# Kernel optimization log

Measured on AMD Instinct MI355X. Metric: run time of the kernel, lower is better.

The kernel has to match this reference:

```python
import jax, jax.numpy as jnp
import numpy as np

DIM = 1024
HEADS = 16
DIM_HEAD = 64
INNER = HEADS * DIM_HEAD  # 1024


def setup_inputs() -> dict:
    key = jax.random.key(0)
    kx, kqkv, kwo, kbo = jax.random.split(key, 4)
    x = jax.random.normal(kx, (4, 2048, DIM), dtype=jnp.float32)
    # nn.Linear weights stored as [out, in]; we keep [in, out] for x @ W
    w_qkv = jax.random.normal(kqkv, (DIM, 3 * INNER), dtype=jnp.float32) * (1.0 / np.sqrt(DIM))
    w_out = jax.random.normal(kwo, (INNER, DIM), dtype=jnp.float32) * (1.0 / np.sqrt(INNER))
    b_out = jax.random.normal(kbo, (DIM,), dtype=jnp.float32) * 0.01
    return {"x": x, "w_qkv": w_qkv, "w_out": w_out, "b_out": b_out}


def reference(x, w_qkv, w_out, b_out):
    b, n, _ = x.shape
    scale = 1.0 / np.sqrt(DIM_HEAD)
    qkv = x @ w_qkv  # [b, n, 3*inner]
    q, k, v = jnp.split(qkv, 3, axis=-1)
    # [b, n, inner] -> [b, h, n, d]
    reshape = lambda z: z.reshape(b, n, HEADS, DIM_HEAD).transpose(0, 2, 1, 3)
    q, k, v = reshape(q), reshape(k), reshape(v)
    sim = jnp.einsum('bhid,bhjd->bhij', q, k) * scale
    attn = jax.nn.softmax(sim, axis=-1)  # dropout p=0.0 -> identity
    out = jnp.einsum('bhij,bhjd->bhid', attn, v)
    out = out.transpose(0, 2, 1, 3).reshape(b, n, INNER)
    return out @ w_out + b_out
```

## Files before the change

### kernel.cpp

```cpp
#include <hip/hip_runtime.h>
#include <hip/hip_fp16.h>

typedef __attribute__((ext_vector_type(4))) float f32x4;
typedef __attribute__((ext_vector_type(8))) _Float16 h8;
typedef __attribute__((ext_vector_type(4))) _Float16 h4;
typedef __attribute__((ext_vector_type(2))) _Float16 h2;
typedef __attribute__((ext_vector_type(2))) __fp16 fp16x2;

__device__ __forceinline__ void gld16(const _Float16* g, _Float16* l) {
  __builtin_amdgcn_global_load_lds(
      (const __attribute__((address_space(1))) void*)g,
      (__attribute__((address_space(3))) void*)l, 16, 0, 0);
}

__device__ __forceinline__ h4 pack4(float p0, float p1, float p2, float p3) {
  fp16x2 lo = __builtin_amdgcn_cvt_pkrtz(p0, p1);
  fp16x2 hi = __builtin_amdgcn_cvt_pkrtz(p2, p3);
  h2 lo2 = __builtin_bit_cast(h2, lo);
  h2 hi2 = __builtin_bit_cast(h2, hi);
  return __builtin_shufflevector(lo2, hi2, 0, 1, 2, 3);
}

__global__ void cvt_f32_h(const float* __restrict__ in, _Float16* __restrict__ out, int n8) {
  for (int i = blockIdx.x * blockDim.x + threadIdx.x; i < n8; i += gridDim.x * blockDim.x) {
    const f32x4* p = (const f32x4*)(in + (size_t)i * 8);
    f32x4 a = p[0], b = p[1];
    h8 o;
    o[0] = (_Float16)a[0]; o[1] = (_Float16)a[1]; o[2] = (_Float16)a[2]; o[3] = (_Float16)a[3];
    o[4] = (_Float16)b[0]; o[5] = (_Float16)b[1]; o[6] = (_Float16)b[2]; o[7] = (_Float16)b[3];
    *(h8*)(out + (size_t)i * 8) = o;
  }
}

__global__ void transpose_cvt(const float* __restrict__ in, _Float16* __restrict__ out, int R, int C) {
  __shared__ float tile[32][33];
  const int tx = threadIdx.x & 31, ty = threadIdx.x >> 5;
  const int c = blockIdx.x * 32 + tx;
#pragma unroll
  for (int j = 0; j < 32; j += 8) {
    int r = blockIdx.y * 32 + ty + j;
    tile[ty + j][tx] = in[(size_t)r * C + c];
  }
  __syncthreads();
#pragma unroll
  for (int j = 0; j < 32; j += 8) {
    out[(size_t)(blockIdx.x * 32 + ty + j) * R + blockIdx.y * 32 + tx] = (_Float16)tile[tx][ty + j];
  }
}

template <int EPI>
__global__ __launch_bounds__(256, 2)
void gemm_kernel(const _Float16* __restrict__ A, const _Float16* __restrict__ Bt,
                 float* __restrict__ outF, const float* __restrict__ bias,
                 _Float16* __restrict__ q_h, _Float16* __restrict__ k_h,
                 _Float16* __restrict__ v_t, const int Nn, const int K) {
  __shared__ _Float16 As[128 * 64];
  __shared__ _Float16 Bs[128 * 64];
  const int tid = threadIdx.x;
  const int wid = tid >> 6, lane = tid & 63;
  const int g = lane >> 4, r16 = lane & 15;
  const int wr = wid >> 1, wc = wid & 1;
  const int row0 = blockIdx.x * 128;
  const int col0 = blockIdx.y * 128;
  f32x4 acc[4][4] = {};
  const int sr = tid >> 3, sc = tid & 7;
  const _Float16* ag = A + (size_t)(row0 + sr) * K + sc * 8;
  const _Float16* bg = Bt + (size_t)(col0 + sr) * K + sc * 8;

  for (int kt = 0; kt < K; kt += 64) {
    __syncthreads();
#pragma unroll
    for (int i = 0; i < 4; ++i)
      gld16(ag + (size_t)i * 32 * K + kt, As + i * 2048 + wid * 512);
#pragma unroll
    for (int i = 0; i < 4; ++i)
      gld16(bg + (size_t)i * 32 * K + kt, Bs + i * 2048 + wid * 512);
    __syncthreads();

#pragma unroll
    for (int kk = 0; kk < 2; ++kk) {
      h8 af[4], bf[4];
#pragma unroll
      for (int mt = 0; mt < 4; ++mt)
        af[mt] = *(const h8*)(As + (wr * 64 + mt * 16 + r16) * 64 + kk * 32 + g * 8);
#pragma unroll
      for (int nt = 0; nt < 4; ++nt)
        bf[nt] = *(const h8*)(Bs + (wc * 64 + nt * 16 + r16) * 64 + kk * 32 + g * 8);
#pragma unroll
      for (int mt = 0; mt < 4; ++mt)
#pragma unroll
        for (int nt = 0; nt < 4; ++nt)
          acc[mt][nt] = __builtin_amdgcn_mfma_f32_16x16x32_f16(af[mt], bf[nt], acc[mt][nt], 0, 0, 0);
    }
  }

  if (EPI == 0) {
    const float qscale = 0.125f * 1.44269504088896340736f;
#pragma unroll
    for (int mt = 0; mt < 4; ++mt) {
#pragma unroll
      for (int nt = 0; nt < 4; ++nt) {
        const int j = col0 + wc * 64 + nt * 16 + r16;
        const int which = j >> 10;
        const int hd = j & 1023;
        const int hh = hd >> 6, dd = hd & 63;
#pragma unroll
        for (int rg = 0; rg < 4; ++rg) {
          const int mm = row0 + wr * 64 + mt * 16 + g * 4 + rg;
          const int b = mm >> 11, n = mm & 2047;
          const size_t bh = (size_t)(b * 16 + hh);
          const float v = acc[mt][nt][rg];
          if (which == 0)      q_h[(bh * 2048 + n) * 64 + dd] = (_Float16)(v * qscale);
          else if (which == 1) k_h[(bh * 2048 + n) * 64 + dd] = (_Float16)v;
          else                 v_t[(bh * 64 + dd) * 2048 + n] = (_Float16)v;
        }
      }
    }
  } else {
#pragma unroll
    for (int mt = 0; mt < 4; ++mt) {
#pragma unroll
      for (int nt = 0; nt < 4; ++nt) {
        const int j = col0 + wc * 64 + nt * 16 + r16;
        const float bv = bias[j];
#pragma unroll
        for (int rg = 0; rg < 4; ++rg) {
          const int mm = row0 + wr * 64 + mt * 16 + g * 4 + rg;
          outF[(size_t)mm * Nn + j] = acc[mt][nt][rg] + bv;
        }
      }
    }
  }
}

__device__ __forceinline__ void stage_kv(const _Float16* Kg, const _Float16* Vg,
                                         _Float16* KsB, _Float16* VsB,
                                         int kv0, int sr, int sc8, int wid) {
#pragma unroll
  for (int i = 0; i < 2; ++i) {
    int r = i * 32 + sr;
    gld16(Kg + (size_t)(kv0 + r) * 64 + (sc8 ^ ((r & 7) * 8)), KsB + i * 2048 + wid * 512);
    gld16(Vg + (size_t)r * 2048 + kv0 + (sc8 ^ ((r & 7) * 8)), VsB + i * 2048 + wid * 512);
  }
}

__global__ __launch_bounds__(256, 2)
void attn_kernel(const _Float16* __restrict__ Qall, const _Float16* __restrict__ Kall,
                 const _Float16* __restrict__ Vtall, _Float16* __restrict__ Oall) {
  __shared__ _Float16 Qs[256 * 64];
  __shared__ _Float16 Ks[2][64 * 64];
  __shared__ _Float16 Vs[2][64 * 64];
  const int tid = threadIdx.x;
  const int wid = tid >> 6, lane = tid & 63;
  const int g = lane >> 4, r16 = lane & 15;
  const int blk = (blockIdx.x & 7) * 64 + (blockIdx.x >> 3);
  const int qt = blk & 7;
  const int bh = blk >> 3;
  const _Float16* Qg = Qall + (size_t)bh * (2048 * 64);
  const _Float16* Kg = Kall + (size_t)bh * (2048 * 64);
  const _Float16* Vg = Vtall + (size_t)bh * (2048 * 64);
  const int q0 = qt * 256;
  const int sr = tid >> 3, sc8 = (tid & 7) * 8;

#pragma unroll
  for (int i = 0; i < 8; ++i) {
    int r = i * 32 + sr;
    gld16(Qg + (size_t)(q0 + r) * 64 + (sc8 ^ ((r & 7) * 8)), Qs + i * 2048 + wid * 512);
  }
  stage_kv(Kg, Vg, Ks[0], Vs[0], 0, sr, sc8, wid);
  __syncthreads();

  h8 qf[4][2];
#pragma unroll
  for (int qb = 0; qb < 4; ++qb) {
    const int qrow = wid * 64 + qb * 16 + r16;
#pragma unroll
    for (int kd = 0; kd < 2; ++kd)
      qf[qb][kd] = *(const h8*)(Qs + qrow * 64 + ((kd * 32 + g * 8) ^ ((qrow & 7) * 8)));
  }

  f32x4 ot[4][4] = {};
  f32x4 lacc[4] = {};
  float m[4];
#pragma unroll
  for (int qb = 0; qb < 4; ++qb) m[qb] = -3.0e38f;
  const h4 ones = {(_Float16)1.f, (_Float16)1.f, (_Float16)1.f, (_Float16)1.f};

  auto compute = [&](const _Float16* KsB, const _Float16* VsB) {
    h8 kf[4][2];
#pragma unroll
    for (int kb = 0; kb < 4; ++kb) {
      const int krow = kb * 16 + r16;
#pragma unroll
      for (int kd = 0; kd < 2; ++kd)
        kf[kb][kd] = *(const h8*)(KsB + krow * 64 + ((kd * 32 + g * 8) ^ ((krow & 7) * 8)));
    }
    h4 vf[4][4];
#pragma unroll
    for (int db = 0; db < 4; ++db) {
      const int vrow = db * 16 + r16;
#pragma unroll
      for (int kg = 0; kg < 4; ++kg)
        vf[db][kg] = *(const h4*)(VsB + vrow * 64 + ((kg * 16 + g * 4) ^ ((vrow & 7) * 8)));
    }
#pragma unroll
    for (int qb = 0; qb < 4; ++qb) {
      f32x4 st[4];
#pragma unroll
      for (int kb = 0; kb < 4; ++kb) {
        f32x4 z = {};
        st[kb] = __builtin_amdgcn_mfma_f32_16x16x32_f16(kf[kb][0], qf[qb][0], z, 0, 0, 0);
      }
#pragma unroll
      for (int kb = 0; kb < 4; ++kb)
        st[kb] = __builtin_amdgcn_mfma_f32_16x16x32_f16(kf[kb][1], qf[qb][1], st[kb], 0, 0, 0);

      float a0 = fmaxf(fmaxf(st[0][0], st[0][1]), fmaxf(st[0][2], st[0][3]));
      float a1 = fmaxf(fmaxf(st[1][0], st[1][1]), fmaxf(st[1][2], st[1][3]));
      float a2 = fmaxf(fmaxf(st[2][0], st[2][1]), fmaxf(st[2][2], st[2][3]));
      float a3 = fmaxf(fmaxf(st[3][0], st[3][1]), fmaxf(st[3][2], st[3][3]));
      float pmax = fmaxf(fmaxf(a0, a1), fmaxf(a2, a3));
      pmax = fmaxf(pmax, __shfl_xor(pmax, 16));
      pmax = fmaxf(pmax, __shfl_xor(pmax, 32));
      if (__any(pmax > m[qb] + 8.f)) {
        const float mn = fmaxf(m[qb], pmax);
        const float corr = __builtin_amdgcn_exp2f(m[qb] - mn);
        lacc[qb] *= corr;
#pragma unroll
        for (int db = 0; db < 4; ++db) ot[qb][db] *= corr;
        m[qb] = mn;
      }
      h4 pb[4];
#pragma unroll
      for (int kb = 0; kb < 4; ++kb) {
        float p0 = __builtin_amdgcn_exp2f(st[kb][0] - m[qb]);
        float p1 = __builtin_amdgcn_exp2f(st[kb][1] - m[qb]);
        float p2 = __builtin_amdgcn_exp2f(st[kb][2] - m[qb]);
        float p3 = __builtin_amdgcn_exp2f(st[kb][3] - m[qb]);
        pb[kb] = pack4(p0, p1, p2, p3);
      }
#pragma unroll
      for (int kg = 0; kg < 4; ++kg) {
#pragma unroll
        for (int db = 0; db < 4; ++db)
          ot[qb][db] = __builtin_amdgcn_mfma_f32_16x16x16f16(vf[db][kg], pb[kg], ot[qb][db], 0, 0, 0);
        lacc[qb] = __builtin_amdgcn_mfma_f32_16x16x16f16(ones, pb[kg], lacc[qb], 0, 0, 0);
      }
    }
  };

#pragma unroll 1
  for (int tt = 0; tt < 16; ++tt) {
    stage_kv(Kg, Vg, Ks[1], Vs[1], (tt * 2 + 1) * 64, sr, sc8, wid);
    compute(Ks[0], Vs[0]);
    __syncthreads();
    if (tt < 15) stage_kv(Kg, Vg, Ks[0], Vs[0], (tt * 2 + 2) * 64, sr, sc8, wid);
    compute(Ks[1], Vs[1]);
    __syncthreads();
  }

#pragma unroll
  for (int qb = 0; qb < 4; ++qb) {
    const float inv = 1.f / lacc[qb][0];
    const int qrow = wid * 64 + qb * 16 + r16;
    const int x = (qrow & 7) * 8;
#pragma unroll
    for (int db = 0; db < 4; ++db) {
      h4 o;
#pragma unroll
      for (int rg = 0; rg < 4; ++rg) o[rg] = (_Float16)(ot[qb][db][rg] * inv);
      *(h4*)(Qs + qrow * 64 + ((db * 16 + g * 4) ^ x)) = o;
    }
  }
  __syncthreads();
  const int bb = bh >> 4, hh = bh & 15;
#pragma unroll
  for (int i = 0; i < 8; ++i) {
    const int idx = tid + i * 256;
    const int q = idx >> 3, c = idx & 7;
    h8 vv = *(const h8*)(Qs + q * 64 + ((c * 8) ^ ((q & 7) * 8)));
    *(h8*)(Oall + ((size_t)(bb * 2048 + q0 + q) * 1024 + hh * 64 + c * 8)) = vv;
  }
}

extern "C" void kernel_launch(void* const* d_in, const int* in_sizes, int n_in,
                              void* d_out, int out_size, void* d_ws, size_t ws_size,
                              hipStream_t stream) {
  const float* x     = (const float*)d_in[0];
  const float* w_qkv = (const float*)d_in[1];
  const float* w_out = (const float*)d_in[2];
  const float* b_out = (const float*)d_in[3];
  float* out = (float*)d_out;

  char* ws = (char*)d_ws;
  _Float16* x_h    = (_Float16*)(ws);
  _Float16* wqkv_t = (_Float16*)(ws + 16777216);
  _Float16* wout_t = (_Float16*)(ws + 23068672);
  _Float16* q_h    = (_Float16*)(ws + 25165824);
  _Float16* k_h    = (_Float16*)(ws + 41943040);
  _Float16* v_t    = (_Float16*)(ws + 58720256);
  _Float16* o_h    = (_Float16*)(ws + 75497472);

  hipLaunchKernelGGL(cvt_f32_h, dim3(2048), dim3(256), 0, stream, x, x_h, (8192 * 1024) / 8);
  hipLaunchKernelGGL(transpose_cvt, dim3(96, 32), dim3(256), 0, stream, w_qkv, wqkv_t, 1024, 3072);
  hipLaunchKernelGGL(transpose_cvt, dim3(32, 32), dim3(256), 0, stream, w_out, wout_t, 1024, 1024);

  hipLaunchKernelGGL((gemm_kernel<0>), dim3(64, 24), dim3(256), 0, stream,
                     x_h, wqkv_t, nullptr, nullptr, q_h, k_h, v_t, 3072, 1024);

  hipLaunchKernelGGL(attn_kernel, dim3(512), dim3(256), 0, stream, q_h, k_h, v_t, o_h);

  hipLaunchKernelGGL((gemm_kernel<1>), dim3(64, 8), dim3(256), 0, stream,
                     o_h, wout_t, out, b_out, nullptr, nullptr, nullptr, 1024, 1024);
}
```

Measured before the change: 230.3 us.

## Halve attention query tile and drop Q shared staging to raise occupancy

The attention kernel now processes 128 query rows per block (32 per wave) instead of 256, and launches 1024 blocks. Q fragments are loaded directly from global memory into registers, so shared memory shrinks to the K/V double buffers, which are reused for the output staging. The row sum is now computed with shuffles instead of an extra MFMA against a ones vector, and launch bounds ask for 4 blocks per CU. This is meant to raise occupancy and parallelism, but each block now reuses each K/V tile across fewer query rows, so K/V traffic per unit of work doubles.

```diff
diff --git a/kernel.cpp b/kernel.cpp
--- a/kernel.cpp
+++ b/kernel.cpp
@@ -144,47 +144,35 @@
   }
 }
 
-__global__ __launch_bounds__(256, 2)
+__global__ __launch_bounds__(256, 4)
 void attn_kernel(const _Float16* __restrict__ Qall, const _Float16* __restrict__ Kall,
                  const _Float16* __restrict__ Vtall, _Float16* __restrict__ Oall) {
-  __shared__ _Float16 Qs[256 * 64];
-  __shared__ _Float16 Ks[2][64 * 64];
-  __shared__ _Float16 Vs[2][64 * 64];
+  __shared__ _Float16 smem[2][2][64 * 64];
   const int tid = threadIdx.x;
   const int wid = tid >> 6, lane = tid & 63;
   const int g = lane >> 4, r16 = lane & 15;
-  const int blk = (blockIdx.x & 7) * 64 + (blockIdx.x >> 3);
-  const int qt = blk & 7;
-  const int bh = blk >> 3;
+  const int blk = (blockIdx.x & 7) * 128 + (blockIdx.x >> 3);
+  const int qt = blk & 15;
+  const int bh = blk >> 4;
   const _Float16* Qg = Qall + (size_t)bh * (2048 * 64);
   const _Float16* Kg = Kall + (size_t)bh * (2048 * 64);
   const _Float16* Vg = Vtall + (size_t)bh * (2048 * 64);
-  const int q0 = qt * 256;
+  const int q0 = qt * 128;
   const int sr = tid >> 3, sc8 = (tid & 7) * 8;
 
-#pragma unroll
-  for (int i = 0; i < 8; ++i) {
-    int r = i * 32 + sr;
-    gld16(Qg + (size_t)(q0 + r) * 64 + (sc8 ^ ((r & 7) * 8)), Qs + i * 2048 + wid * 512);
-  }
-  stage_kv(Kg, Vg, Ks[0], Vs[0], 0, sr, sc8, wid);
+  h8 qf[2][2];
+#pragma unroll
+  for (int qb = 0; qb < 2; ++qb) {
+    const int qrow = q0 + wid * 32 + qb * 16 + r16;
+#pragma unroll
+    for (int kd = 0; kd < 2; ++kd)
+      qf[qb][kd] = *(const h8*)(Qg + (size_t)qrow * 64 + kd * 32 + g * 8);
+  }
+  stage_kv(Kg, Vg, smem[0][0], smem[0][1], 0, sr, sc8, wid);
   __syncthreads();
 
-  h8 qf[4][2];
-#pragma unroll
-  for (int qb = 0; qb < 4; ++qb) {
-    const int qrow = wid * 64 + qb * 16 + r16;
-#pragma unroll
-    for (int kd = 0; kd < 2; ++kd)
-      qf[qb][kd] = *(const h8*)(Qs + qrow * 64 + ((kd * 32 + g * 8) ^ ((qrow & 7) * 8)));
-  }
-
-  f32x4 ot[4][4] = {};
-  f32x4 lacc[4] = {};
-  float m[4];
-#pragma unroll
-  for (int qb = 0; qb < 4; ++qb) m[qb] = -3.0e38f;
-  const h4 ones = {(_Float16)1.f, (_Float16)1.f, (_Float16)1.f, (_Float16)1.f};
+  f32x4 ot[2][4] = {};
+  float m[2] = {-3.0e38f, -3.0e38f}, l[2] = {0.f, 0.f};
 
   auto compute = [&](const _Float16* KsB, const _Float16* VsB) {
     h8 kf[4][2];
@@ -204,7 +192,7 @@
         vf[db][kg] = *(const h4*)(VsB + vrow * 64 + ((kg * 16 + g * 4) ^ ((vrow & 7) * 8)));
     }
 #pragma unroll
-    for (int qb = 0; qb < 4; ++qb) {
+    for (int qb = 0; qb < 2; ++qb) {
       f32x4 st[4];
 #pragma unroll
       for (int kb = 0; kb < 4; ++kb) {
@@ -225,11 +213,12 @@
       if (__any(pmax > m[qb] + 8.f)) {
         const float mn = fmaxf(m[qb], pmax);
         const float corr = __builtin_amdgcn_exp2f(m[qb] - mn);
-        lacc[qb] *= corr;
+        l[qb] *= corr;
 #pragma unroll
         for (int db = 0; db < 4; ++db) ot[qb][db] *= corr;
         m[qb] = mn;
       }
+      float rs = 0.f;
       h4 pb[4];
 #pragma unroll
       for (int kb = 0; kb < 4; ++kb) {
@@ -237,48 +226,51 @@
         float p1 = __builtin_amdgcn_exp2f(st[kb][1] - m[qb]);
         float p2 = __builtin_amdgcn_exp2f(st[kb][2] - m[qb]);
         float p3 = __builtin_amdgcn_exp2f(st[kb][3] - m[qb]);
+        rs += (p0 + p1) + (p2 + p3);
         pb[kb] = pack4(p0, p1, p2, p3);
       }
-#pragma unroll
-      for (int kg = 0; kg < 4; ++kg) {
+      rs += __shfl_xor(rs, 16);
+      rs += __shfl_xor(rs, 32);
+      l[qb] += rs;
+#pragma unroll
+      for (int kg = 0; kg < 4; ++kg)
 #pragma unroll
         for (int db = 0; db < 4; ++db)
           ot[qb][db] = __builtin_amdgcn_mfma_f32_16x16x16f16(vf[db][kg], pb[kg], ot[qb][db], 0, 0, 0);
-        lacc[qb] = __builtin_amdgcn_mfma_f32_16x16x16f16(ones, pb[kg], lacc[qb], 0, 0, 0);
-      }
     }
   };
 
 #pragma unroll 1
   for (int tt = 0; tt < 16; ++tt) {
-    stage_kv(Kg, Vg, Ks[1], Vs[1], (tt * 2 + 1) * 64, sr, sc8, wid);
-    compute(Ks[0], Vs[0]);
+    stage_kv(Kg, Vg, smem[1][0], smem[1][1], (tt * 2 + 1) * 64, sr, sc8, wid);
+    compute(smem[0][0], smem[0][1]);
     __syncthreads();
-    if (tt < 15) stage_kv(Kg, Vg, Ks[0], Vs[0], (tt * 2 + 2) * 64, sr, sc8, wid);
-    compute(Ks[1], Vs[1]);
+    if (tt < 15) stage_kv(Kg, Vg, smem[0][0], smem[0][1], (tt * 2 + 2) * 64, sr, sc8, wid);
+    compute(smem[1][0], smem[1][1]);
     __syncthreads();
   }
 
-#pragma unroll
-  for (int qb = 0; qb < 4; ++qb) {
-    const float inv = 1.f / lacc[qb][0];
-    const int qrow = wid * 64 + qb * 16 + r16;
+  _Float16* olds = &smem[0][0][0];
+#pragma unroll
+  for (int qb = 0; qb < 2; ++qb) {
+    const float inv = 1.f / l[qb];
+    const int qrow = wid * 32 + qb * 16 + r16;
     const int x = (qrow & 7) * 8;
 #pragma unroll
     for (int db = 0; db < 4; ++db) {
       h4 o;
 #pragma unroll
       for (int rg = 0; rg < 4; ++rg) o[rg] = (_Float16)(ot[qb][db][rg] * inv);
-      *(h4*)(Qs + qrow * 64 + ((db * 16 + g * 4) ^ x)) = o;
+      *(h4*)(olds + qrow * 64 + ((db * 16 + g * 4) ^ x)) = o;
     }
   }
   __syncthreads();
   const int bb = bh >> 4, hh = bh & 15;
 #pragma unroll
-  for (int i = 0; i < 8; ++i) {
+  for (int i = 0; i < 4; ++i) {
     const int idx = tid + i * 256;
     const int q = idx >> 3, c = idx & 7;
-    h8 vv = *(const h8*)(Qs + q * 64 + ((c * 8) ^ ((q & 7) * 8)));
+    h8 vv = *(const h8*)(olds + q * 64 + ((c * 8) ^ ((q & 7) * 8)));
     *(h8*)(Oall + ((size_t)(bb * 2048 + q0 + q) * 1024 + hh * 64 + c * 8)) = vv;
   }
 }
@@ -308,7 +300,7 @@
   hipLaunchKernelGGL((gemm_kernel<0>), dim3(64, 24), dim3(256), 0, stream,
                      x_h, wqkv_t, nullptr, nullptr, q_h, k_h, v_t, 3072, 1024);
 
-  hipLaunchKernelGGL(attn_kernel, dim3(512), dim3(256), 0, stream, q_h, k_h, v_t, o_h);
+  hipLaunchKernelGGL(attn_kernel, dim3(1024), dim3(256), 0, stream, q_h, k_h, v_t, o_h);
 
   hipLaunchKernelGGL((gemm_kernel<1>), dim3(64, 8), dim3(256), 0, stream,
                      o_h, wout_t, out, b_out, nullptr, nullptr, nullptr, 1024, 1024);
```

New measurement: 288.8 us. 1.25x slower.
